# Kernel optimization log

Measured on AMD Instinct MI355X. Metric: run time of the kernel, lower is better.

The kernel has to match this reference:

```python
import jax, jax.numpy as jnp
import numpy as np

C, H, W = 4, 512, 512  # featuremap: (C, feature_width, feature_height) -> (C, H_in, W_in)
HID = 16
N = 4_000_000


def _lin_init(key, fan_in, fan_out):
    kw, kb = jax.random.split(key)
    bound = 1.0 / np.sqrt(fan_in)
    Wm = jax.random.uniform(kw, (fan_in, fan_out), jnp.float32, -bound, bound)
    b = jax.random.uniform(kb, (fan_out,), jnp.float32, -bound, bound)
    return Wm, b


def setup_inputs() -> dict:
    key = jax.random.key(0)
    ks = jax.random.split(key, 7)
    x = jax.random.uniform(ks[0], (N, 3), jnp.float32)
    featuremap = 0.1 * jax.random.normal(ks[1], (C, H, W), jnp.float32)
    W1, b1 = _lin_init(ks[2], 7, HID)
    W2, b2 = _lin_init(ks[3], HID, HID)
    W3, b3 = _lin_init(ks[4], HID, HID)
    W4, b4 = _lin_init(ks[5], HID, HID)
    W5, b5 = _lin_init(ks[6], HID, 3)
    return {"x": x, "featuremap": featuremap, "W1": W1, "b1": b1, "W2": W2,
            "b2": b2, "W3": W3, "b3": b3, "W4": W4, "b4": b4, "W5": W5, "b5": b5}


def _grid_sample_border(fm, uv):
    # fm: [C, H_in, W_in]; uv: [N, 2] in [0,1], col0 -> width (x), col1 -> height (y)
    # matches F.grid_sample(mode='bilinear', padding_mode='border', align_corners=False)
    c, h, w = fm.shape
    g = uv * 2.0 - 1.0
    fx = jnp.clip(((g[:, 0] + 1.0) * w - 1.0) * 0.5, 0.0, w - 1.0)
    fy = jnp.clip(((g[:, 1] + 1.0) * h - 1.0) * 0.5, 0.0, h - 1.0)
    x0 = jnp.floor(fx)
    y0 = jnp.floor(fy)
    wx1 = fx - x0
    wy1 = fy - y0
    ix0 = x0.astype(jnp.int32)
    iy0 = y0.astype(jnp.int32)
    ix1 = jnp.minimum(ix0 + 1, w - 1)
    iy1 = jnp.minimum(iy0 + 1, h - 1)
    v00 = fm[:, iy0, ix0]  # [C, N]
    v01 = fm[:, iy0, ix1]
    v10 = fm[:, iy1, ix0]
    v11 = fm[:, iy1, ix1]
    out = (v00 * ((1.0 - wy1) * (1.0 - wx1)) + v01 * ((1.0 - wy1) * wx1)
           + v10 * (wy1 * (1.0 - wx1)) + v11 * (wy1 * wx1))
    return out.T  # [N, C]


def reference(x, featuremap, W1, b1, W2, b2, W3, b3, W4, b4, W5, b5):
    feat = _grid_sample_border(featuremap, x[:, :2])  # [N, 4]
    h = jnp.concatenate([x, feat], axis=-1)           # [N, 7]
    h = jax.nn.relu(h @ W1 + b1)
    h = jax.nn.relu(h @ W2 + b2)
    h = jax.nn.relu(h @ W3 + b3)
    h = jax.nn.relu(h @ W4 + b4)
    return h @ W5 + b5
```

## Files before the change

### kernel.cpp

```cpp
#include <hip/hip_runtime.h>

#define HH 512
#define WW 512
#define HWSZ (HH * WW)
#define BLK 256

#define SW1 20
#define O_W1 0
#define O_B1 140
#define O_W2 156
#define O_B2 476
#define O_W3 492
#define O_B3 812
#define O_W4 828
#define O_B4 1148
#define O_W5 1164
#define O_B5 1228
#define SWF_TOT 1244

typedef __fp16 f16x2 __attribute__((ext_vector_type(2)));
typedef __fp16 f16x4 __attribute__((ext_vector_type(4)));
typedef float f32x4 __attribute__((ext_vector_type(4)));

#define MFMA16(a, b, c) __builtin_amdgcn_mfma_f32_16x16x16f16((a), (b), (c), 0, 0, 0)

__device__ inline unsigned pk2u(float a, float b) {
    f16x2 p;
    p[0] = (__fp16)a;
    p[1] = (__fp16)b;
    return __builtin_bit_cast(unsigned, p);
}

__device__ inline f16x4 relu_pack(f32x4 d) {
    f16x4 r;
    r[0] = (__fp16)fmaxf(d[0], 0.f);
    r[1] = (__fp16)fmaxf(d[1], 0.f);
    r[2] = (__fp16)fmaxf(d[2], 0.f);
    r[3] = (__fp16)fmaxf(d[3], 0.f);
    return r;
}

__global__ void fm_transpose_h(const float* __restrict__ fm, f16x4* __restrict__ fmT) {
    int i = blockIdx.x * blockDim.x + threadIdx.x;
    if (i < HWSZ) {
        f16x4 v;
        v[0] = (__fp16)fm[i];
        v[1] = (__fp16)fm[HWSZ + i];
        v[2] = (__fp16)fm[2 * HWSZ + i];
        v[3] = (__fp16)fm[3 * HWSZ + i];
        fmT[i] = v;
    }
}

template <bool TR>
__global__ __launch_bounds__(BLK) void mlp_fused(
    const float* __restrict__ x, const void* __restrict__ fmv,
    const float* __restrict__ W1, const float* __restrict__ b1,
    const float* __restrict__ W2, const float* __restrict__ b2,
    const float* __restrict__ W3, const float* __restrict__ b3,
    const float* __restrict__ W4, const float* __restrict__ b4,
    const float* __restrict__ W5, const float* __restrict__ b5,
    float* __restrict__ out, int n)
{
    __shared__ __align__(16) float sW[SWF_TOT];
    __shared__ __align__(16) unsigned sX[BLK * 4];
    const int tid = threadIdx.x;

    if (tid < 112) { int r = tid >> 4, c = tid & 15; sW[O_W1 + r * SW1 + c] = W1[tid]; }
    if (tid < 16) {
        sW[O_B1 + tid] = b1[tid];
        sW[O_B2 + tid] = b2[tid];
        sW[O_B3 + tid] = b3[tid];
        sW[O_B4 + tid] = b4[tid];
        sW[O_B5 + tid] = (tid < 3) ? b5[tid] : 0.f;
    }
    {
        int r = tid >> 4, c = tid & 15;
        sW[O_W2 + r * SW1 + c] = W2[tid];
        sW[O_W3 + r * SW1 + c] = W3[tid];
        sW[O_W4 + r * SW1 + c] = W4[tid];
    }
    if (tid < 48) { int r = tid / 3, c = tid % 3; sW[O_W5 + r * 4 + c] = W5[tid]; }

    const int i = blockIdx.x * BLK + tid;
    const int ii = (i < n) ? i : (n - 1);

    float p0 = x[3 * ii], p1 = x[3 * ii + 1], p2 = x[3 * ii + 2];

    float gx = p0 * 2.f - 1.f;
    float gy = p1 * 2.f - 1.f;
    float fx = ((gx + 1.f) * (float)WW - 1.f) * 0.5f;
    float fy = ((gy + 1.f) * (float)HH - 1.f) * 0.5f;
    fx = fminf(fmaxf(fx, 0.f), (float)(WW - 1));
    fy = fminf(fmaxf(fy, 0.f), (float)(HH - 1));
    float x0f = floorf(fx), y0f = floorf(fy);
    float wx = fx - x0f, wy = fy - y0f;
    int ix0 = (int)x0f, iy0 = (int)y0f;
    int ix1 = min(ix0 + 1, WW - 1);
    int iy1 = min(iy0 + 1, HH - 1);
    float w00 = (1.f - wy) * (1.f - wx);
    float w01 = (1.f - wy) * wx;
    float w10 = wy * (1.f - wx);
    float w11 = wy * wx;

    float feat[4];
    if (TR) {
        const f16x4* fmH = reinterpret_cast<const f16x4*>(fmv);
        f16x4 h00 = fmH[iy0 * WW + ix0];
        f16x4 h01 = fmH[iy0 * WW + ix1];
        f16x4 h10 = fmH[iy1 * WW + ix0];
        f16x4 h11 = fmH[iy1 * WW + ix1];
#pragma unroll
        for (int ch = 0; ch < 4; ++ch) {
            feat[ch] = (float)h00[ch] * w00 + (float)h01[ch] * w01 +
                       (float)h10[ch] * w10 + (float)h11[ch] * w11;
        }
    } else {
        const float* fmf = reinterpret_cast<const float*>(fmv);
#pragma unroll
        for (int ch = 0; ch < 4; ++ch) {
            const float* f = fmf + ch * HWSZ;
            feat[ch] = f[iy0 * WW + ix0] * w00 + f[iy0 * WW + ix1] * w01 +
                       f[iy1 * WW + ix0] * w10 + f[iy1 * WW + ix1] * w11;
        }
    }

    {
        uint4 rec;
        rec.x = pk2u(p0, p1);
        rec.y = pk2u(p2, feat[0]);
        rec.z = pk2u(feat[1], feat[2]);
        rec.w = pk2u(feat[3], 0.f);
        reinterpret_cast<uint4*>(sX)[tid] = rec;
    }
    __syncthreads();

    const int lane = tid & 63;
    const int wv = tid >> 6;
    const int jj = lane & 15;
    const int kg = lane >> 4;

    f16x4 A1, A2, A3, A4, A5;
#pragma unroll
    for (int e = 0; e < 4; ++e) {
        int k = 4 * kg + e;
        A1[e] = (__fp16)((k < 7) ? sW[O_W1 + k * SW1 + jj] : 0.f);
        A2[e] = (__fp16)sW[O_W2 + k * SW1 + jj];
        A3[e] = (__fp16)sW[O_W3 + k * SW1 + jj];
        A4[e] = (__fp16)sW[O_W4 + k * SW1 + jj];
        A5[e] = (__fp16)((jj < 3) ? sW[O_W5 + k * 4 + jj] : 0.f);
    }
    f32x4 C1 = *reinterpret_cast<const f32x4*>(sW + O_B1 + 4 * kg);
    f32x4 C2 = *reinterpret_cast<const f32x4*>(sW + O_B2 + 4 * kg);
    f32x4 C3 = *reinterpret_cast<const f32x4*>(sW + O_B3 + 4 * kg);
    f32x4 C4 = *reinterpret_cast<const f32x4*>(sW + O_B4 + 4 * kg);
    f32x4 C5 = *reinterpret_cast<const f32x4*>(sW + O_B5 + 4 * kg);

    f16x4 B0, B1f, B2f, B3f;
    {
        const int pb = wv * 64;
#define LOADB(Bv, g)                                                         \
        {                                                                    \
            uint2 raw = make_uint2(0u, 0u);                                  \
            if (kg < 2)                                                      \
                raw = *reinterpret_cast<const uint2*>(                       \
                    sX + (pb + (g) * 16 + jj) * 4 + kg * 2);                 \
            (Bv) = __builtin_bit_cast(f16x4, raw);                           \
        }
        LOADB(B0, 0) LOADB(B1f, 1) LOADB(B2f, 2) LOADB(B3f, 3)
#undef LOADB
    }

    f32x4 D0, D1, D2, D3;
    D0 = MFMA16(A1, B0, C1);  D1 = MFMA16(A1, B1f, C1);
    D2 = MFMA16(A1, B2f, C1); D3 = MFMA16(A1, B3f, C1);
    B0 = relu_pack(D0); B1f = relu_pack(D1); B2f = relu_pack(D2); B3f = relu_pack(D3);
    D0 = MFMA16(A2, B0, C2);  D1 = MFMA16(A2, B1f, C2);
    D2 = MFMA16(A2, B2f, C2); D3 = MFMA16(A2, B3f, C2);
    B0 = relu_pack(D0); B1f = relu_pack(D1); B2f = relu_pack(D2); B3f = relu_pack(D3);
    D0 = MFMA16(A3, B0, C3);  D1 = MFMA16(A3, B1f, C3);
    D2 = MFMA16(A3, B2f, C3); D3 = MFMA16(A3, B3f, C3);
    B0 = relu_pack(D0); B1f = relu_pack(D1); B2f = relu_pack(D2); B3f = relu_pack(D3);
    D0 = MFMA16(A4, B0, C4);  D1 = MFMA16(A4, B1f, C4);
    D2 = MFMA16(A4, B2f, C4); D3 = MFMA16(A4, B3f, C4);
    B0 = relu_pack(D0); B1f = relu_pack(D1); B2f = relu_pack(D2); B3f = relu_pack(D3);
    D0 = MFMA16(A5, B0, C5);  D1 = MFMA16(A5, B1f, C5);
    D2 = MFMA16(A5, B2f, C5); D3 = MFMA16(A5, B3f, C5);

    if (kg == 0) {
        const int gbase = blockIdx.x * BLK + wv * 64 + jj;
#define STOREG(Dv, g)                                                        \
        {                                                                    \
            int gp = gbase + (g) * 16;                                       \
            if (gp < n) {                                                    \
                out[3 * gp]     = (Dv)[0];                                   \
                out[3 * gp + 1] = (Dv)[1];                                   \
                out[3 * gp + 2] = (Dv)[2];                                   \
            }                                                                \
        }
        STOREG(D0, 0) STOREG(D1, 1) STOREG(D2, 2) STOREG(D3, 3)
#undef STOREG
    }
}

extern "C" void kernel_launch(void* const* d_in, const int* in_sizes, int n_in,
                              void* d_out, int out_size, void* d_ws, size_t ws_size,
                              hipStream_t stream) {
    const float* x  = (const float*)d_in[0];
    const float* fm = (const float*)d_in[1];
    const float* W1 = (const float*)d_in[2];
    const float* b1 = (const float*)d_in[3];
    const float* W2 = (const float*)d_in[4];
    const float* b2 = (const float*)d_in[5];
    const float* W3 = (const float*)d_in[6];
    const float* b3 = (const float*)d_in[7];
    const float* W4 = (const float*)d_in[8];
    const float* b4 = (const float*)d_in[9];
    const float* W5 = (const float*)d_in[10];
    const float* b5 = (const float*)d_in[11];
    float* out = (float*)d_out;

    const int n = in_sizes[0] / 3;
    const int grid = (n + BLK - 1) / BLK;

    const size_t need = (size_t)HWSZ * sizeof(f16x4);
    if (ws_size >= need) {
        f16x4* fmT = (f16x4*)d_ws;
        fm_transpose_h<<<(HWSZ + 255) / 256, 256, 0, stream>>>(fm, fmT);
        mlp_fused<true><<<grid, BLK, 0, stream>>>(x, (const void*)fmT, W1, b1,
                                                  W2, b2, W3, b3, W4, b4, W5, b5,
                                                  out, n);
    } else {
        mlp_fused<false><<<grid, BLK, 0, stream>>>(x, (const void*)fm, W1, b1,
                                                   W2, b2, W3, b3, W4, b4, W5, b5,
                                                   out, n);
    }
}
```

Baseline: 164.5 us.

## Process multiple tiles per block with software-pipelined gather and MLP

Each block now handles TPB=8 tiles of 256 points instead of one. A double-buffered shared-memory staging area lets the featuremap gather and x loads for upcoming tiles be issued while the MFMA chain runs on the current tile. This amortises the per-block weight loading and tries to hide gather latency behind compute. The cost is more live registers, which may lower occupancy, fewer blocks in the grid, and a serial loop carrying one barrier per tile.

```diff
diff --git a/kernel.cpp b/kernel.cpp
--- a/kernel.cpp
+++ b/kernel.cpp
@@ -4,6 +4,7 @@
 #define WW 512
 #define HWSZ (HH * WW)
 #define BLK 256
+#define TPB 8
 
 #define SW1 20
 #define O_W1 0
@@ -63,7 +64,7 @@
     float* __restrict__ out, int n)
 {
     __shared__ __align__(16) float sW[SWF_TOT];
-    __shared__ __align__(16) unsigned sX[BLK * 4];
+    __shared__ __align__(16) unsigned sX[2][BLK * 4];
     const int tid = threadIdx.x;
 
     if (tid < 112) { int r = tid >> 4, c = tid & 15; sW[O_W1 + r * SW1 + c] = W1[tid]; }
@@ -82,65 +83,140 @@
     }
     if (tid < 48) { int r = tid / 3, c = tid % 3; sW[O_W5 + r * 4 + c] = W5[tid]; }
 
-    const int i = blockIdx.x * BLK + tid;
-    const int ii = (i < n) ? i : (n - 1);
-
-    float p0 = x[3 * ii], p1 = x[3 * ii + 1], p2 = x[3 * ii + 2];
-
-    float gx = p0 * 2.f - 1.f;
-    float gy = p1 * 2.f - 1.f;
-    float fx = ((gx + 1.f) * (float)WW - 1.f) * 0.5f;
-    float fy = ((gy + 1.f) * (float)HH - 1.f) * 0.5f;
-    fx = fminf(fmaxf(fx, 0.f), (float)(WW - 1));
-    fy = fminf(fmaxf(fy, 0.f), (float)(HH - 1));
-    float x0f = floorf(fx), y0f = floorf(fy);
-    float wx = fx - x0f, wy = fy - y0f;
-    int ix0 = (int)x0f, iy0 = (int)y0f;
-    int ix1 = min(ix0 + 1, WW - 1);
-    int iy1 = min(iy0 + 1, HH - 1);
-    float w00 = (1.f - wy) * (1.f - wx);
-    float w01 = (1.f - wy) * wx;
-    float w10 = wy * (1.f - wx);
-    float w11 = wy * wx;
-
-    float feat[4];
-    if (TR) {
-        const f16x4* fmH = reinterpret_cast<const f16x4*>(fmv);
-        f16x4 h00 = fmH[iy0 * WW + ix0];
-        f16x4 h01 = fmH[iy0 * WW + ix1];
-        f16x4 h10 = fmH[iy1 * WW + ix0];
-        f16x4 h11 = fmH[iy1 * WW + ix1];
-#pragma unroll
-        for (int ch = 0; ch < 4; ++ch) {
-            feat[ch] = (float)h00[ch] * w00 + (float)h01[ch] * w01 +
-                       (float)h10[ch] * w10 + (float)h11[ch] * w11;
-        }
-    } else {
-        const float* fmf = reinterpret_cast<const float*>(fmv);
-#pragma unroll
-        for (int ch = 0; ch < 4; ++ch) {
-            const float* f = fmf + ch * HWSZ;
-            feat[ch] = f[iy0 * WW + ix0] * w00 + f[iy0 * WW + ix1] * w01 +
-                       f[iy1 * WW + ix0] * w10 + f[iy1 * WW + ix1] * w11;
-        }
-    }
-
-    {
-        uint4 rec;
-        rec.x = pk2u(p0, p1);
-        rec.y = pk2u(p2, feat[0]);
-        rec.z = pk2u(feat[1], feat[2]);
-        rec.w = pk2u(feat[3], 0.f);
-        reinterpret_cast<uint4*>(sX)[tid] = rec;
-    }
-    __syncthreads();
-
     const int lane = tid & 63;
     const int wv = tid >> 6;
     const int jj = lane & 15;
     const int kg = lane >> 4;
+    const int tile0 = blockIdx.x * TPB;
+
+    const f16x4* fmH = reinterpret_cast<const f16x4*>(fmv);
+    const float* fmf = reinterpret_cast<const float*>(fmv);
+
+    float pa0, pa1, pa2;
+    float pb0, pb1, pb2;
+    uint2 gv00, gv01, gv10, gv11;
+
+    auto loadX = [&](int t, float& q0, float& q1, float& q2) {
+        int p = (tile0 + t) * BLK + tid;
+        int ii = (p < n) ? p : (n - 1);
+        q0 = x[3 * ii]; q1 = x[3 * ii + 1]; q2 = x[3 * ii + 2];
+    };
+    auto addr = [&](float q0, float q1, int& ix0, int& iy0, int& ix1, int& iy1,
+                    float& wxo, float& wyo) {
+        float gx = q0 * 2.f - 1.f;
+        float gy = q1 * 2.f - 1.f;
+        float fx = ((gx + 1.f) * (float)WW - 1.f) * 0.5f;
+        float fy = ((gy + 1.f) * (float)HH - 1.f) * 0.5f;
+        fx = fminf(fmaxf(fx, 0.f), (float)(WW - 1));
+        fy = fminf(fmaxf(fy, 0.f), (float)(HH - 1));
+        float x0f = floorf(fx), y0f = floorf(fy);
+        wxo = fx - x0f; wyo = fy - y0f;
+        ix0 = (int)x0f; iy0 = (int)y0f;
+        ix1 = min(ix0 + 1, WW - 1);
+        iy1 = min(iy0 + 1, HH - 1);
+    };
+    auto issueG = [&](float q0, float q1) {
+        if (TR) {
+            int ix0, iy0, ix1, iy1; float wxo, wyo;
+            addr(q0, q1, ix0, iy0, ix1, iy1, wxo, wyo);
+            const uint2* f2 = reinterpret_cast<const uint2*>(fmH);
+            gv00 = f2[iy0 * WW + ix0];
+            gv01 = f2[iy0 * WW + ix1];
+            gv10 = f2[iy1 * WW + ix0];
+            gv11 = f2[iy1 * WW + ix1];
+        }
+    };
+    auto interpPackWrite = [&](float q0, float q1, float q2, int buf) {
+        int ix0, iy0, ix1, iy1; float wxo, wyo;
+        addr(q0, q1, ix0, iy0, ix1, iy1, wxo, wyo);
+        float w00 = (1.f - wyo) * (1.f - wxo);
+        float w01 = (1.f - wyo) * wxo;
+        float w10 = wyo * (1.f - wxo);
+        float w11 = wyo * wxo;
+        float feat[4];
+        if (TR) {
+            f16x4 v00 = __builtin_bit_cast(f16x4, gv00);
+            f16x4 v01 = __builtin_bit_cast(f16x4, gv01);
+            f16x4 v10 = __builtin_bit_cast(f16x4, gv10);
+            f16x4 v11 = __builtin_bit_cast(f16x4, gv11);
+#pragma unroll
+            for (int ch = 0; ch < 4; ++ch) {
+                feat[ch] = (float)v00[ch] * w00 + (float)v01[ch] * w01 +
+                           (float)v10[ch] * w10 + (float)v11[ch] * w11;
+            }
+        } else {
+#pragma unroll
+            for (int ch = 0; ch < 4; ++ch) {
+                const float* f = fmf + ch * HWSZ;
+                feat[ch] = f[iy0 * WW + ix0] * w00 + f[iy0 * WW + ix1] * w01 +
+                           f[iy1 * WW + ix0] * w10 + f[iy1 * WW + ix1] * w11;
+            }
+        }
+        uint4 rec;
+        rec.x = pk2u(q0, q1);
+        rec.y = pk2u(q2, feat[0]);
+        rec.z = pk2u(feat[1], feat[2]);
+        rec.w = pk2u(feat[3], 0.f);
+        reinterpret_cast<uint4*>(sX[buf])[tid] = rec;
+    };
 
     f16x4 A1, A2, A3, A4, A5;
+    f32x4 C1, C2, C3, C4, C5;
+
+    auto runTile = [&](int t, int buf) {
+        const unsigned* sxb = sX[buf];
+        f16x4 B0, B1f, B2f, B3f;
+        const int pb = wv * 64;
+#define LOADB(Bv, g)                                                         \
+        {                                                                    \
+            uint2 raw = make_uint2(0u, 0u);                                  \
+            if (kg < 2)                                                      \
+                raw = *reinterpret_cast<const uint2*>(                       \
+                    sxb + (pb + (g) * 16 + jj) * 4 + kg * 2);                \
+            (Bv) = __builtin_bit_cast(f16x4, raw);                           \
+        }
+        LOADB(B0, 0) LOADB(B1f, 1) LOADB(B2f, 2) LOADB(B3f, 3)
+#undef LOADB
+        f32x4 D0, D1, D2, D3;
+        D0 = MFMA16(A1, B0, C1);  D1 = MFMA16(A1, B1f, C1);
+        D2 = MFMA16(A1, B2f, C1); D3 = MFMA16(A1, B3f, C1);
+        B0 = relu_pack(D0); B1f = relu_pack(D1); B2f = relu_pack(D2); B3f = relu_pack(D3);
+        D0 = MFMA16(A2, B0, C2);  D1 = MFMA16(A2, B1f, C2);
+        D2 = MFMA16(A2, B2f, C2); D3 = MFMA16(A2, B3f, C2);
+        B0 = relu_pack(D0); B1f = relu_pack(D1); B2f = relu_pack(D2); B3f = relu_pack(D3);
+        D0 = MFMA16(A3, B0, C3);  D1 = MFMA16(A3, B1f, C3);
+        D2 = MFMA16(A3, B2f, C3); D3 = MFMA16(A3, B3f, C3);
+        B0 = relu_pack(D0); B1f = relu_pack(D1); B2f = relu_pack(D2); B3f = relu_pack(D3);
+        D0 = MFMA16(A4, B0, C4);  D1 = MFMA16(A4, B1f, C4);
+        D2 = MFMA16(A4, B2f, C4); D3 = MFMA16(A4, B3f, C4);
+        B0 = relu_pack(D0); B1f = relu_pack(D1); B2f = relu_pack(D2); B3f = relu_pack(D3);
+        D0 = MFMA16(A5, B0, C5);  D1 = MFMA16(A5, B1f, C5);
+        D2 = MFMA16(A5, B2f, C5); D3 = MFMA16(A5, B3f, C5);
+        if (kg == 0) {
+            const int gbase = (tile0 + t) * BLK + wv * 64 + jj;
+#define STOREG(Dv, g)                                                        \
+            {                                                                \
+                int gp = gbase + (g) * 16;                                   \
+                if (gp < n) {                                                \
+                    out[3 * gp]     = (Dv)[0];                               \
+                    out[3 * gp + 1] = (Dv)[1];                               \
+                    out[3 * gp + 2] = (Dv)[2];                               \
+                }                                                            \
+            }
+            STOREG(D0, 0) STOREG(D1, 1) STOREG(D2, 2) STOREG(D3, 3)
+#undef STOREG
+        }
+    };
+
+    {
+        float q0, q1, q2;
+        loadX(0, q0, q1, q2);
+        issueG(q0, q1);
+        interpPackWrite(q0, q1, q2, 0);
+    }
+    loadX(1, pa0, pa1, pa2);
+    __syncthreads();
+
 #pragma unroll
     for (int e = 0; e < 4; ++e) {
         int k = 4 * kg + e;
@@ -150,56 +226,23 @@
         A4[e] = (__fp16)sW[O_W4 + k * SW1 + jj];
         A5[e] = (__fp16)((jj < 3) ? sW[O_W5 + k * 4 + jj] : 0.f);
     }
-    f32x4 C1 = *reinterpret_cast<const f32x4*>(sW + O_B1 + 4 * kg);
-    f32x4 C2 = *reinterpret_cast<const f32x4*>(sW + O_B2 + 4 * kg);
-    f32x4 C3 = *reinterpret_cast<const f32x4*>(sW + O_B3 + 4 * kg);
-    f32x4 C4 = *reinterpret_cast<const f32x4*>(sW + O_B4 + 4 * kg);
-    f32x4 C5 = *reinterpret_cast<const f32x4*>(sW + O_B5 + 4 * kg);
-
-    f16x4 B0, B1f, B2f, B3f;
-    {
-        const int pb = wv * 64;
-#define LOADB(Bv, g)                                                         \
-        {                                                                    \
-            uint2 raw = make_uint2(0u, 0u);                                  \
-            if (kg < 2)                                                      \
-                raw = *reinterpret_cast<const uint2*>(                       \
-                    sX + (pb + (g) * 16 + jj) * 4 + kg * 2);                 \
-            (Bv) = __builtin_bit_cast(f16x4, raw);                           \
-        }
-        LOADB(B0, 0) LOADB(B1f, 1) LOADB(B2f, 2) LOADB(B3f, 3)
-#undef LOADB
-    }
-
-    f32x4 D0, D1, D2, D3;
-    D0 = MFMA16(A1, B0, C1);  D1 = MFMA16(A1, B1f, C1);
-    D2 = MFMA16(A1, B2f, C1); D3 = MFMA16(A1, B3f, C1);
-    B0 = relu_pack(D0); B1f = relu_pack(D1); B2f = relu_pack(D2); B3f = relu_pack(D3);
-    D0 = MFMA16(A2, B0, C2);  D1 = MFMA16(A2, B1f, C2);
-    D2 = MFMA16(A2, B2f, C2); D3 = MFMA16(A2, B3f, C2);
-    B0 = relu_pack(D0); B1f = relu_pack(D1); B2f = relu_pack(D2); B3f = relu_pack(D3);
-    D0 = MFMA16(A3, B0, C3);  D1 = MFMA16(A3, B1f, C3);
-    D2 = MFMA16(A3, B2f, C3); D3 = MFMA16(A3, B3f, C3);
-    B0 = relu_pack(D0); B1f = relu_pack(D1); B2f = relu_pack(D2); B3f = relu_pack(D3);
-    D0 = MFMA16(A4, B0, C4);  D1 = MFMA16(A4, B1f, C4);
-    D2 = MFMA16(A4, B2f, C4); D3 = MFMA16(A4, B3f, C4);
-    B0 = relu_pack(D0); B1f = relu_pack(D1); B2f = relu_pack(D2); B3f = relu_pack(D3);
-    D0 = MFMA16(A5, B0, C5);  D1 = MFMA16(A5, B1f, C5);
-    D2 = MFMA16(A5, B2f, C5); D3 = MFMA16(A5, B3f, C5);
-
-    if (kg == 0) {
-        const int gbase = blockIdx.x * BLK + wv * 64 + jj;
-#define STOREG(Dv, g)                                                        \
-        {                                                                    \
-            int gp = gbase + (g) * 16;                                       \
-            if (gp < n) {                                                    \
-                out[3 * gp]     = (Dv)[0];                                   \
-                out[3 * gp + 1] = (Dv)[1];                                   \
-                out[3 * gp + 2] = (Dv)[2];                                   \
-            }                                                                \
-        }
-        STOREG(D0, 0) STOREG(D1, 1) STOREG(D2, 2) STOREG(D3, 3)
-#undef STOREG
+    C1 = *reinterpret_cast<const f32x4*>(sW + O_B1 + 4 * kg);
+    C2 = *reinterpret_cast<const f32x4*>(sW + O_B2 + 4 * kg);
+    C3 = *reinterpret_cast<const f32x4*>(sW + O_B3 + 4 * kg);
+    C4 = *reinterpret_cast<const f32x4*>(sW + O_B4 + 4 * kg);
+    C5 = *reinterpret_cast<const f32x4*>(sW + O_B5 + 4 * kg);
+
+    issueG(pa0, pa1);
+
+#pragma unroll 1
+    for (int t = 0; t < TPB; ++t) {
+        const int cur = t & 1;
+        if (t + 2 < TPB) loadX(t + 2, pb0, pb1, pb2);
+        runTile(t, cur);
+        if (t + 1 < TPB) interpPackWrite(pa0, pa1, pa2, cur ^ 1);
+        pa0 = pb0; pa1 = pb1; pa2 = pb2;
+        __syncthreads();
+        if (t + 2 < TPB) issueG(pa0, pa1);
     }
 }
 
@@ -221,7 +264,8 @@
     float* out = (float*)d_out;
 
     const int n = in_sizes[0] / 3;
-    const int grid = (n + BLK - 1) / BLK;
+    const int tiles = (n + BLK - 1) / BLK;
+    const int grid = (tiles + TPB - 1) / TPB;
 
     const size_t need = (size_t)HWSZ * sizeof(f16x4);
     if (ws_size >= need) {
```

Measured after the change: 166.5 us. Within noise of the previous version (+1.2%).
